# Performance work log

Hardware: AMD Instinct MI355X
Metric: run time of the kernel (lower is better)

## Reference

```python
import jax, jax.numpy as jnp
import numpy as np

C = 512

def _conv1x1(x, w, b):
    # x: [B, C, T], w: [O, C], b: [O] -> [B, O, T]
    return jnp.einsum('oc,bct->bot', w, x) + b[None, :, None]

def setup_inputs() -> dict:
    key = jax.random.key(0)
    ks = jax.random.split(key, 9)
    B, T = 8, 2048
    s = 1.0 / np.sqrt(C)
    inp = {'x': jax.random.normal(ks[0], (B, C, T), dtype=jnp.float32)}
    names = ['theta', 'phi', 'g', 'w']
    for i, n in enumerate(names):
        inp[f'w_{n}'] = jax.random.uniform(ks[1 + 2 * i], (C, C), jnp.float32, -s, s)
        inp[f'b_{n}'] = jax.random.uniform(ks[2 + 2 * i], (C,), jnp.float32, -s, s)
    return inp

def reference(x, w_theta, b_theta, w_phi, b_phi, w_g, b_g, w_w, b_w):
    relu = jax.nn.relu
    feat_theta = relu(_conv1x1(x, w_theta, b_theta))          # [B, C, T]
    feat_phi = relu(_conv1x1(x, w_phi, b_phi))                # [B, C, T]
    # scores: Q^T K over channel dim -> [B, T, T]
    scores = jnp.einsum('bci,bcj->bij', feat_theta, feat_phi)
    attn = jax.nn.softmax(scores, axis=2)                     # [B, T, T]
    feat_g = relu(_conv1x1(x, w_g, b_g))                      # [B, C, T]
    # attention-weighted V: [B, T, T] x [B, T, C] -> [B, T, C] -> [B, C, T]
    feature = jnp.einsum('bij,bcj->bci', attn, feat_g)
    w_feature = relu(_conv1x1(feature, w_w, b_w))
    return w_feature + x
```

## Files before the change

### kernel.cpp

```cpp
#include <hip/hip_runtime.h>
#include <math.h>

#define C_DIM 512
#define T_DIM 2048
#define B_DIM 8

typedef _Float16 f16;
typedef __attribute__((ext_vector_type(8))) _Float16 half8;
typedef __attribute__((ext_vector_type(4))) _Float16 half4;
typedef __attribute__((ext_vector_type(4))) float floatx4;

__global__ __launch_bounds__(256) void convert_w_kernel(
    const float* __restrict__ w0, const float* __restrict__ w1,
    const float* __restrict__ w2, const float* __restrict__ w3,
    f16* __restrict__ o0, f16* __restrict__ o1,
    f16* __restrict__ o2, f16* __restrict__ o3)
{
    const float* src; f16* dst;
    switch (blockIdx.z) {
        case 0:  src = w0; dst = o0; break;
        case 1:  src = w1; dst = o1; break;
        case 2:  src = w2; dst = o2; break;
        default: src = w3; dst = o3; break;
    }
    const int idx = (blockIdx.x * 256 + threadIdx.x) * 4;
    const float4 v = *(const float4*)(src + idx);
    half4 h; h[0] = (f16)v.x; h[1] = (f16)v.y; h[2] = (f16)v.z; h[3] = (f16)v.w;
    *(half4*)(dst + idx) = h;
}

__global__ __launch_bounds__(256) void concat_bias_kernel(
    const float* __restrict__ b0, const float* __restrict__ b1,
    float* __restrict__ o)
{
    const int i = blockIdx.x * 256 + threadIdx.x;
    o[i] = (i < 512) ? b0[i] : b1[i - 512];
}

__global__ __launch_bounds__(256) void transpose_x_kernel(
    const float* __restrict__ x, f16* __restrict__ xt)
{
    __shared__ float xs[32][33];
    const int b  = blockIdx.z;
    const int t0 = blockIdx.x * 32, c0 = blockIdx.y * 32;
    const float* xb = x + (size_t)b * C_DIM * T_DIM;
    const int r = threadIdx.x >> 3, q = threadIdx.x & 7;

    const float4 v = *(const float4*)(xb + (size_t)(c0 + r) * T_DIM + t0 + q * 4);
    xs[r][q * 4 + 0] = v.x; xs[r][q * 4 + 1] = v.y;
    xs[r][q * 4 + 2] = v.z; xs[r][q * 4 + 3] = v.w;
    __syncthreads();

    f16* xtb = xt + (size_t)b * C_DIM * T_DIM;
    half4 h;
    h[0] = (f16)xs[q * 4 + 0][r]; h[1] = (f16)xs[q * 4 + 1][r];
    h[2] = (f16)xs[q * 4 + 2][r]; h[3] = (f16)xs[q * 4 + 3][r];
    *(half4*)(xtb + (size_t)(t0 + r) * C_DIM + c0 + q * 4) = h;
}

template<int MODE>
__global__ __launch_bounds__(256) void gemm_tn(
    const f16* __restrict__ A, size_t sA, int lda,
    const f16* __restrict__ B, size_t sB, int ldb,
    void* __restrict__ Cp, size_t sC, int ldc,
    const float* __restrict__ bias,
    const float* __restrict__ resid, size_t sR,
    int K)
{
    __shared__ __align__(16) f16 As[2][128 * 32];
    __shared__ __align__(16) f16 Bs[2][128 * 32];

    const int gx = gridDim.x;
    const int flat = blockIdx.y * gx + blockIdx.x;
    const int jsc = gx >> 2;
    const int sh = (jsc <= 1) ? 0 : (31 - __builtin_clz(jsc));
    const int s = flat >> 4, rem = flat & 15;
    const int i0 = ((s >> sh) * 4 + (rem >> 2)) * 128;
    const int j0 = (((jsc <= 1) ? 0 : (s & (jsc - 1))) * 4 + (rem & 3)) * 128;

    const int bz = blockIdx.z;
    A += (size_t)bz * sA;
    B += (size_t)bz * sB;

    const int tid  = threadIdx.x;
    const int lane = tid & 63;
    const int wave = tid >> 6;
    const int wy = wave >> 1, wx = wave & 1;
    const int quad = lane >> 4, l16 = lane & 15;

    const int row1 = tid >> 2, ch = tid & 3;
    const int row2 = row1 + 64;
    const int w1 = row1 * 32 + ((ch ^ (row1 & 3)) << 3);
    const int w2 = row2 * 32 + ((ch ^ (row2 & 3)) << 3);

    const f16* gA1 = A + (size_t)(i0 + row1) * lda + ch * 8;
    const f16* gA2 = A + (size_t)(i0 + row2) * lda + ch * 8;
    const f16* gB1 = B + (size_t)(j0 + row1) * ldb + ch * 8;
    const f16* gB2 = B + (size_t)(j0 + row2) * ldb + ch * 8;

    const int xa = (quad ^ (l16 & 3)) << 3;

    const int nt = K >> 5;

    float4 a1_0 = *(const float4*)(gA1);      float4 a2_0 = *(const float4*)(gA2);
    float4 b1_0 = *(const float4*)(gB1);      float4 b2_0 = *(const float4*)(gB2);
    float4 a1_1 = *(const float4*)(gA1 + 32); float4 a2_1 = *(const float4*)(gA2 + 32);
    float4 b1_1 = *(const float4*)(gB1 + 32); float4 b2_1 = *(const float4*)(gB2 + 32);

    floatx4 acc[4][4] = {};

    for (int t = 0; t < nt; t += 2) {
        *(float4*)&As[0][w1] = a1_0;
        *(float4*)&As[0][w2] = a2_0;
        *(float4*)&Bs[0][w1] = b1_0;
        *(float4*)&Bs[0][w2] = b2_0;
        if (t + 2 < nt) {
            const int off = (t + 2) * 32;
            a1_0 = *(const float4*)(gA1 + off); a2_0 = *(const float4*)(gA2 + off);
            b1_0 = *(const float4*)(gB1 + off); b2_0 = *(const float4*)(gB2 + off);
        }
        __syncthreads();
        {
            half8 af[4], bf[4];
            #pragma unroll
            for (int mi = 0; mi < 4; ++mi)
                af[mi] = *(const half8*)&As[0][(wy * 64 + mi * 16 + l16) * 32 + xa];
            #pragma unroll
            for (int ni = 0; ni < 4; ++ni)
                bf[ni] = *(const half8*)&Bs[0][(wx * 64 + ni * 16 + l16) * 32 + xa];
            #pragma unroll
            for (int mi = 0; mi < 4; ++mi)
                #pragma unroll
                for (int ni = 0; ni < 4; ++ni)
                    acc[mi][ni] = __builtin_amdgcn_mfma_f32_16x16x32_f16(
                        af[mi], bf[ni], acc[mi][ni], 0, 0, 0);
        }
        *(float4*)&As[1][w1] = a1_1;
        *(float4*)&As[1][w2] = a2_1;
        *(float4*)&Bs[1][w1] = b1_1;
        *(float4*)&Bs[1][w2] = b2_1;
        if (t + 3 < nt) {
            const int off = (t + 3) * 32;
            a1_1 = *(const float4*)(gA1 + off); a2_1 = *(const float4*)(gA2 + off);
            b1_1 = *(const float4*)(gB1 + off); b2_1 = *(const float4*)(gB2 + off);
        }
        __syncthreads();
        {
            half8 af[4], bf[4];
            #pragma unroll
            for (int mi = 0; mi < 4; ++mi)
                af[mi] = *(const half8*)&As[1][(wy * 64 + mi * 16 + l16) * 32 + xa];
            #pragma unroll
            for (int ni = 0; ni < 4; ++ni)
                bf[ni] = *(const half8*)&Bs[1][(wx * 64 + ni * 16 + l16) * 32 + xa];
            #pragma unroll
            for (int mi = 0; mi < 4; ++mi)
                #pragma unroll
                for (int ni = 0; ni < 4; ++ni)
                    acc[mi][ni] = __builtin_amdgcn_mfma_f32_16x16x32_f16(
                        af[mi], bf[ni], acc[mi][ni], 0, 0, 0);
        }
    }

    #pragma unroll
    for (int mi = 0; mi < 4; ++mi) {
        #pragma unroll
        for (int ni = 0; ni < 4; ++ni) {
            const int col = j0 + wx * 64 + ni * 16 + l16;
            #pragma unroll
            for (int r = 0; r < 4; ++r) {
                const int row = i0 + wy * 64 + mi * 16 + quad * 4 + r;
                float v = acc[mi][ni][r];
                if (MODE == 1) { v += bias[col]; v = v > 0.f ? v : 0.f; }
                if (MODE == 2) { v += bias[row]; v = v > 0.f ? v : 0.f; }
                if (MODE == 3) {
                    v += bias[row];
                    v = v > 0.f ? v : 0.f;
                    v += resid[(size_t)bz * sR + (size_t)row * ldc + col];
                    ((float*)Cp)[(size_t)bz * sC + (size_t)row * ldc + col] = v;
                } else {
                    ((f16*)Cp)[(size_t)bz * sC + (size_t)row * ldc + col] = (f16)v;
                }
            }
        }
    }
}

__device__ __forceinline__ void gl16(const f16* g, f16* l)
{
    __builtin_amdgcn_global_load_lds(
        (const __attribute__((address_space(1))) unsigned int*)g,
        (__attribute__((address_space(3))) unsigned int*)l,
        16, 0, 0);
}

template<int MODE>
__global__ __launch_bounds__(512, 2) void gemm256(
    const f16* __restrict__ A, size_t sA, int lda,
    const f16* __restrict__ B, size_t sB, int ldb,
    void* __restrict__ Cp, size_t sC, int ldc,
    const float* __restrict__ bias,
    int K)
{
    __shared__ __align__(16) f16 As[2][256 * 32];
    __shared__ __align__(16) f16 Bs[2][256 * 32];

    const int gx = gridDim.x;
    const int flat = blockIdx.y * gx + blockIdx.x;
    const int jsc = gx >> 2;
    const int sh = (jsc <= 1) ? 0 : (31 - __builtin_clz(jsc));
    const int s = flat >> 4, rem = flat & 15;
    const int i0 = ((s >> sh) * 4 + (rem >> 2)) * 256;
    const int j0 = (((jsc <= 1) ? 0 : (s & (jsc - 1))) * 4 + (rem & 3)) * 256;

    const int bz = blockIdx.z;
    A += (size_t)bz * sA;
    B += (size_t)bz * sB;

    const int tid  = threadIdx.x;
    const int lane = tid & 63;
    const int wave = tid >> 6;
    const int wy = wave >> 2;
    const int wx = wave & 3;
    const int quad = lane >> 4, l16 = lane & 15;

    const int srow = wave * 32 + (lane >> 2);
    const int sch  = lane & 3;
    const f16* gAs0 = A + (size_t)(i0 + srow) * lda + sch * 8;
    const f16* gAs1 = gAs0 + (size_t)16 * lda;
    const f16* gBs0 = B + (size_t)(j0 + srow) * ldb + sch * 8;
    const f16* gBs1 = gBs0 + (size_t)16 * ldb;
    const int wsg = wave * 1024;

    const int ra = (wy * 128 + l16) * 32 + quad * 8;
    const int rb = (wx * 64 + l16) * 32 + quad * 8;

    const int nt = K >> 5;

    gl16(gAs0,      &As[0][wsg]); gl16(gAs1,      &As[0][wsg + 512]);
    gl16(gBs0,      &Bs[0][wsg]); gl16(gBs1,      &Bs[0][wsg + 512]);
    gl16(gAs0 + 32, &As[1][wsg]); gl16(gAs1 + 32, &As[1][wsg + 512]);
    gl16(gBs0 + 32, &Bs[1][wsg]); gl16(gBs1 + 32, &Bs[1][wsg + 512]);

    floatx4 acc[8][4] = {};

#define MFMA8(M0, AF0, AF1)                                                   \
    do {                                                                      \
        __builtin_amdgcn_s_setprio(1);                                        \
        _Pragma("unroll")                                                     \
        for (int ni = 0; ni < 4; ++ni)                                        \
            acc[M0][ni] = __builtin_amdgcn_mfma_f32_16x16x32_f16(             \
                AF0, bf[ni], acc[M0][ni], 0, 0, 0);                           \
        _Pragma("unroll")                                                     \
        for (int ni = 0; ni < 4; ++ni)                                        \
            acc[(M0) + 1][ni] = __builtin_amdgcn_mfma_f32_16x16x32_f16(       \
                AF1, bf[ni], acc[(M0) + 1][ni], 0, 0, 0);                     \
        __builtin_amdgcn_s_setprio(0);                                        \
    } while (0)

    for (int t = 0; t < nt; ++t) {
        if (t < nt - 1)
            asm volatile("s_waitcnt vmcnt(4)\ns_barrier" ::: "memory");
        else
            asm volatile("s_waitcnt vmcnt(0)\ns_barrier" ::: "memory");

        const f16* sa = &As[t & 1][0];
        const f16* sb = &Bs[t & 1][0];

        half8 bf[4];
        #pragma unroll
        for (int ni = 0; ni < 4; ++ni)
            bf[ni] = *(const half8*)&sb[rb + ni * 512];

        half8 af0 = *(const half8*)&sa[ra];
        half8 af1 = *(const half8*)&sa[ra + 512];
        MFMA8(0, af0, af1);
        af0 = *(const half8*)&sa[ra + 1024];
        af1 = *(const half8*)&sa[ra + 1536];
        MFMA8(2, af0, af1);
        af0 = *(const half8*)&sa[ra + 2048];
        af1 = *(const half8*)&sa[ra + 2560];
        MFMA8(4, af0, af1);
        af0 = *(const half8*)&sa[ra + 3072];
        af1 = *(const half8*)&sa[ra + 3584];
        MFMA8(6, af0, af1);

        asm volatile("s_barrier" ::: "memory");
        if (t + 2 < nt) {
            const int off = (t + 2) * 32;
            f16* stA = &As[t & 1][wsg];
            f16* stB = &Bs[t & 1][wsg];
            gl16(gAs0 + off, stA); gl16(gAs1 + off, stA + 512);
            gl16(gBs0 + off, stB); gl16(gBs1 + off, stB + 512);
        }
    }
#undef MFMA8

    #pragma unroll
    for (int m = 0; m < 8; ++m) {
        #pragma unroll
        for (int ni = 0; ni < 4; ++ni) {
            const int col = j0 + wx * 64 + ni * 16 + l16;
            #pragma unroll
            for (int r = 0; r < 4; ++r) {
                const int row = i0 + wy * 128 + m * 16 + quad * 4 + r;
                float v = acc[m][ni][r];
                if (MODE == 1) { v += bias[col]; v = v > 0.f ? v : 0.f; }
                ((f16*)Cp)[(size_t)bz * sC + (size_t)row * ldc + col] = (f16)v;
            }
        }
    }
}

__global__ __launch_bounds__(256) void softmax_f16_kernel(f16* __restrict__ S)
{
    f16* p = S + (size_t)blockIdx.x * T_DIM;
    const int tid = threadIdx.x;

    half8 hv = *((const half8*)p + tid);
    float v[8];
    float lmax = -1e30f;
    #pragma unroll
    for (int c = 0; c < 8; ++c) { v[c] = (float)hv[c]; lmax = fmaxf(lmax, v[c]); }
    #pragma unroll
    for (int off = 32; off; off >>= 1)
        lmax = fmaxf(lmax, __shfl_down(lmax, off));
    __shared__ float redm[4];
    if ((tid & 63) == 0) redm[tid >> 6] = lmax;
    __syncthreads();
    const float m = fmaxf(fmaxf(redm[0], redm[1]), fmaxf(redm[2], redm[3]));

    float lsum = 0.f;
    #pragma unroll
    for (int c = 0; c < 8; ++c) { v[c] = __expf(v[c] - m); lsum += v[c]; }
    #pragma unroll
    for (int off = 32; off; off >>= 1)
        lsum += __shfl_down(lsum, off);
    __shared__ float reds[4];
    if ((tid & 63) == 0) reds[tid >> 6] = lsum;
    __syncthreads();
    const float inv = 1.f / (reds[0] + reds[1] + reds[2] + reds[3]);

    #pragma unroll
    for (int c = 0; c < 8; ++c) hv[c] = (f16)(v[c] * inv);
    *((half8*)p + tid) = hv;
}

extern "C" void kernel_launch(void* const* d_in, const int* in_sizes, int n_in,
                              void* d_out, int out_size, void* d_ws, size_t ws_size,
                              hipStream_t stream)
{
    const float* x       = (const float*)d_in[0];
    const float* w_theta = (const float*)d_in[1];
    const float* b_theta = (const float*)d_in[2];
    const float* w_phi   = (const float*)d_in[3];
    const float* b_phi   = (const float*)d_in[4];
    const float* w_g     = (const float*)d_in[5];
    const float* b_g     = (const float*)d_in[6];
    const float* w_w     = (const float*)d_in[7];
    const float* b_w     = (const float*)d_in[8];
    float* out = (float*)d_out;

    const size_t FE = (size_t)B_DIM * C_DIM * T_DIM;
    const size_t TC = (size_t)T_DIM * C_DIM;
    const size_t TT = (size_t)T_DIM * T_DIM;

    f16* xt      = (f16*)d_ws;
    f16* wtp     = xt + FE;
    f16* wg_h    = wtp + 524288;
    f16* ww_h    = wg_h + 262144;
    float* btp   = (float*)(ww_h + 262144);
    f16* tp      = (f16*)(btp + 1024);
    f16* g       = tp + (size_t)B_DIM * T_DIM * 1024;
    f16* scores  = g + FE;
    f16* feature = tp;

    const dim3 blk(256);
    const dim3 blk512(512);

    convert_w_kernel<<<dim3(256, 1, 4), blk, 0, stream>>>(
        w_theta, w_phi, w_g, w_w, wtp, wtp + 262144, wg_h, ww_h);
    concat_bias_kernel<<<dim3(4), blk, 0, stream>>>(b_theta, b_phi, btp);
    transpose_x_kernel<<<dim3(T_DIM / 32, C_DIM / 32, B_DIM), blk, 0, stream>>>(x, xt);

    gemm256<1><<<dim3(1024 / 256, T_DIM / 256, B_DIM), blk512, 0, stream>>>(
        xt, TC, C_DIM, wtp, 0, C_DIM, tp, (size_t)T_DIM * 1024, 1024,
        btp, C_DIM);
    gemm_tn<2><<<dim3(T_DIM / 128, C_DIM / 128, B_DIM), blk, 0, stream>>>(
        wg_h, 0, C_DIM, xt, TC, C_DIM, g, TC, T_DIM, b_g, nullptr, 0, C_DIM);
    gemm256<0><<<dim3(T_DIM / 256, T_DIM / 256, B_DIM), blk512, 0, stream>>>(
        tp, (size_t)T_DIM * 1024, 1024, tp + 512, (size_t)T_DIM * 1024, 1024,
        scores, TT, T_DIM, nullptr, C_DIM);
    softmax_f16_kernel<<<dim3(B_DIM * T_DIM), blk, 0, stream>>>(scores);
    gemm_tn<0><<<dim3(C_DIM / 128, T_DIM / 128, B_DIM), blk, 0, stream>>>(
        scores, TT, T_DIM, g, TC, T_DIM, feature, TC, C_DIM, nullptr, nullptr, 0, T_DIM);
    gemm_tn<3><<<dim3(T_DIM / 128, C_DIM / 128, B_DIM), blk, 0, stream>>>(
        ww_h, 0, C_DIM, feature, TC, C_DIM, out, TC, T_DIM, b_w, x, TC, C_DIM);
}
```

Before: 290.6 us.

## Restructure GEMM main loop into two-half K=64 steps with finer-grained prefetch

The 256x256 f16 GEMM now consumes K in steps of 64, split into two 32-wide halves. Each half has its own LDS buffer, so shared memory per block doubles to 128 KB. Global-to-LDS loads for the next halves are issued between MFMA phases, with vmcnt waits and barriers placed at each half boundary. The aim is better overlap of loads with MFMA work and fewer barrier stalls. The risk is that the doubled LDS footprint allows only one block per CU, which would undo the two-block occupancy the launch bounds request.

```diff
diff --git a/kernel.cpp b/kernel.cpp
--- a/kernel.cpp
+++ b/kernel.cpp
@@ -202,8 +202,8 @@
     const float* __restrict__ bias,
     int K)
 {
-    __shared__ __align__(16) f16 As[2][256 * 32];
-    __shared__ __align__(16) f16 Bs[2][256 * 32];
+    __shared__ __align__(16) f16 As[2][2][256 * 32];
+    __shared__ __align__(16) f16 Bs[2][2][256 * 32];
 
     const int gx = gridDim.x;
     const int flat = blockIdx.y * gx + blockIdx.x;
@@ -226,75 +226,83 @@
 
     const int srow = wave * 32 + (lane >> 2);
     const int sch  = lane & 3;
-    const f16* gAs0 = A + (size_t)(i0 + srow) * lda + sch * 8;
-    const f16* gAs1 = gAs0 + (size_t)16 * lda;
-    const f16* gBs0 = B + (size_t)(j0 + srow) * ldb + sch * 8;
-    const f16* gBs1 = gBs0 + (size_t)16 * ldb;
+    const f16* gA0 = A + (size_t)(i0 + srow) * lda + sch * 8;
+    const f16* gA1 = gA0 + (size_t)16 * lda;
+    const f16* gB0 = B + (size_t)(j0 + srow) * ldb + sch * 8;
+    const f16* gB1 = gB0 + (size_t)16 * ldb;
     const int wsg = wave * 1024;
 
     const int ra = (wy * 128 + l16) * 32 + quad * 8;
     const int rb = (wx * 64 + l16) * 32 + quad * 8;
 
-    const int nt = K >> 5;
-
-    gl16(gAs0,      &As[0][wsg]); gl16(gAs1,      &As[0][wsg + 512]);
-    gl16(gBs0,      &Bs[0][wsg]); gl16(gBs1,      &Bs[0][wsg + 512]);
-    gl16(gAs0 + 32, &As[1][wsg]); gl16(gAs1 + 32, &As[1][wsg + 512]);
-    gl16(gBs0 + 32, &Bs[1][wsg]); gl16(gBs1 + 32, &Bs[1][wsg + 512]);
-
-    floatx4 acc[8][4] = {};
-
-#define MFMA8(M0, AF0, AF1)                                                   \
-    do {                                                                      \
+    const int nt = K >> 6;
+
+#define STAGE_A(t, q) do {                                                    \
+        const int off_ = (t) * 64 + (q) * 32;                                 \
+        gl16(gA0 + off_, &As[(t) & 1][q][wsg]);                               \
+        gl16(gA1 + off_, &As[(t) & 1][q][wsg + 512]);                         \
+    } while (0)
+#define STAGE_B(t, q) do {                                                    \
+        const int off_ = (t) * 64 + (q) * 32;                                 \
+        gl16(gB0 + off_, &Bs[(t) & 1][q][wsg]);                               \
+        gl16(gB1 + off_, &Bs[(t) & 1][q][wsg + 512]);                         \
+    } while (0)
+#define PH_MFMA(B0) do {                                                      \
         __builtin_amdgcn_s_setprio(1);                                        \
         _Pragma("unroll")                                                     \
-        for (int ni = 0; ni < 4; ++ni)                                        \
-            acc[M0][ni] = __builtin_amdgcn_mfma_f32_16x16x32_f16(             \
-                AF0, bf[ni], acc[M0][ni], 0, 0, 0);                           \
-        _Pragma("unroll")                                                     \
-        for (int ni = 0; ni < 4; ++ni)                                        \
-            acc[(M0) + 1][ni] = __builtin_amdgcn_mfma_f32_16x16x32_f16(       \
-                AF1, bf[ni], acc[(M0) + 1][ni], 0, 0, 0);                     \
+        for (int mi = 0; mi < 4; ++mi) {                                      \
+            _Pragma("unroll")                                                 \
+            for (int ni = 0; ni < 4; ++ni)                                    \
+                acc[(B0) + mi][ni] = __builtin_amdgcn_mfma_f32_16x16x32_f16(  \
+                    af[mi], bf[ni], acc[(B0) + mi][ni], 0, 0, 0);             \
+        }                                                                     \
         __builtin_amdgcn_s_setprio(0);                                        \
     } while (0)
 
+    STAGE_A(0, 0); STAGE_B(0, 0);
+    STAGE_A(0, 1); STAGE_B(0, 1);
+    STAGE_A(1, 0); STAGE_B(1, 0);
+
+    floatx4 acc[8][4] = {};
+
     for (int t = 0; t < nt; ++t) {
-        if (t < nt - 1)
-            asm volatile("s_waitcnt vmcnt(4)\ns_barrier" ::: "memory");
-        else
-            asm volatile("s_waitcnt vmcnt(0)\ns_barrier" ::: "memory");
-
-        const f16* sa = &As[t & 1][0];
-        const f16* sb = &Bs[t & 1][0];
-
-        half8 bf[4];
-        #pragma unroll
-        for (int ni = 0; ni < 4; ++ni)
-            bf[ni] = *(const half8*)&sb[rb + ni * 512];
-
-        half8 af0 = *(const half8*)&sa[ra];
-        half8 af1 = *(const half8*)&sa[ra + 512];
-        MFMA8(0, af0, af1);
-        af0 = *(const half8*)&sa[ra + 1024];
-        af1 = *(const half8*)&sa[ra + 1536];
-        MFMA8(2, af0, af1);
-        af0 = *(const half8*)&sa[ra + 2048];
-        af1 = *(const half8*)&sa[ra + 2560];
-        MFMA8(4, af0, af1);
-        af0 = *(const half8*)&sa[ra + 3072];
-        af1 = *(const half8*)&sa[ra + 3584];
-        MFMA8(6, af0, af1);
-
-        asm volatile("s_barrier" ::: "memory");
-        if (t + 2 < nt) {
-            const int off = (t + 2) * 32;
-            f16* stA = &As[t & 1][wsg];
-            f16* stB = &Bs[t & 1][wsg];
-            gl16(gAs0 + off, stA); gl16(gAs1 + off, stA + 512);
-            gl16(gBs0 + off, stB); gl16(gBs1 + off, stB + 512);
-        }
+        const f16* sa0 = &As[t & 1][0][0];
+        const f16* sb0 = &Bs[t & 1][0][0];
+        const f16* sa1 = &As[t & 1][1][0];
+        const f16* sb1 = &Bs[t & 1][1][0];
+        half8 af[4], bf[4];
+
+        if (t + 1 < nt) asm volatile("s_waitcnt vmcnt(8)\ns_barrier" ::: "memory");
+        else            asm volatile("s_waitcnt vmcnt(4)\ns_barrier" ::: "memory");
+        #pragma unroll
+        for (int ni = 0; ni < 4; ++ni) bf[ni] = *(const half8*)&sb0[rb + ni * 512];
+        #pragma unroll
+        for (int mi = 0; mi < 4; ++mi) af[mi] = *(const half8*)&sa0[ra + mi * 512];
+        if (t + 1 < nt) STAGE_A(t + 1, 1);
+        PH_MFMA(0);
+
+        #pragma unroll
+        for (int mi = 0; mi < 4; ++mi) af[mi] = *(const half8*)&sa0[ra + 2048 + mi * 512];
+        if (t + 1 < nt) STAGE_B(t + 1, 1);
+        PH_MFMA(4);
+
+        if (t + 1 < nt) asm volatile("s_waitcnt vmcnt(8)\ns_barrier" ::: "memory");
+        else            asm volatile("s_waitcnt vmcnt(0)\ns_barrier" ::: "memory");
+        #pragma unroll
+        for (int ni = 0; ni < 4; ++ni) bf[ni] = *(const half8*)&sb1[rb + ni * 512];
+        #pragma unroll
+        for (int mi = 0; mi < 4; ++mi) af[mi] = *(const half8*)&sa1[ra + mi * 512];
+        if (t + 2 < nt) STAGE_A(t + 2, 0);
+        PH_MFMA(0);
+
+        #pragma unroll
+        for (int mi = 0; mi < 4; ++mi) af[mi] = *(const half8*)&sa1[ra + 2048 + mi * 512];
+        if (t + 2 < nt) STAGE_B(t + 2, 0);
+        PH_MFMA(4);
     }
-#undef MFMA8
+#undef STAGE_A
+#undef STAGE_B
+#undef PH_MFMA
 
     #pragma unroll
     for (int m = 0; m < 8; ++m) {
```

After: 270.0 us. -7.1%, faster.
